# Performance work log

Hardware: AMD Instinct MI355X
Metric: run time of the kernel (lower is better)

The kernel has to match this reference:

```python
import jax, jax.numpy as jnp
import numpy as np

EPS = 1e-16
LOG_2PI = float(np.log(2.0 * np.pi))
DUMMY = -2.0 * float(np.log(10.0))  # dummy component logit / log-prob


def setup_inputs() -> dict:
    key = jax.random.key(0)
    k1, k2, k3, k4, k5 = jax.random.split(key, 5)
    B, N, V, D = 32, 1024, 512, 4
    x = jax.random.normal(k1, (B, N, D), dtype=jnp.float32)
    votes = jax.random.normal(k2, (B, V, D), dtype=jnp.float32)
    # positive stds in [0.1, 1.0)
    scales = jax.random.uniform(k3, (B, V), dtype=jnp.float32) * 0.9 + 0.1
    vote_presence_prob = jax.random.uniform(k4, (B, V), dtype=jnp.float32)
    presence = jax.random.uniform(k5, (B, N), dtype=jnp.float32)
    return {"x": x, "votes": votes, "scales": scales,
            "vote_presence_prob": vote_presence_prob,
            "presence": presence, "n_votes": 16}


def reference(x, votes, scales, vote_presence_prob, presence, n_votes):
    B, N, D = x.shape
    V = votes.shape[1]
    # Broadcast Normal log-prob: x [B,N,1,D] vs votes [B,1,V,D], scale [B,1,V,1]
    sig = scales[:, None, :, None]
    z = (x[:, :, None, :] - votes[:, None, :, :]) / sig
    lp_per_dim = -0.5 * z * z - jnp.log(sig) - 0.5 * LOG_2PI
    vote_log_prob = jnp.sum(lp_per_dim, axis=-1)                       # [B,N,V]
    vote_log_prob = jnp.concatenate(
        [vote_log_prob, jnp.full((B, N, 1), DUMMY, vote_log_prob.dtype)], axis=2)  # [B,N,V+1]

    mixing_logits = jnp.log(vote_presence_prob + EPS)                  # safe_log, [B,V]
    mixing_logits = jnp.concatenate(
        [mixing_logits, jnp.full((B, 1), DUMMY, mixing_logits.dtype)], axis=1)     # [B,V+1]
    mixing_log_prob = jax.nn.log_softmax(mixing_logits, axis=1)        # [B,V+1]

    posterior = mixing_log_prob[:, None, :] + vote_log_prob            # [B,N,V+1]
    mixture_lp_per_comp = jax.scipy.special.logsumexp(posterior, axis=2)  # [B,N]
    mixture_lp_per_comp = mixture_lp_per_comp * presence
    log_prob = jnp.sum(mixture_lp_per_comp)                            # scalar

    winning_vote_idx = jnp.argmax(posterior[:, :, :-1], axis=2)        # [B,N]
    winner = jnp.take_along_axis(votes, winning_vote_idx[:, :, None], axis=1)  # [B,N,D]
    winner_pres = jnp.take_along_axis(vote_presence_prob, winning_vote_idx, axis=1)  # [B,N]
    vote_presence = (mixing_logits[:, :-1] > mixing_logits[:, -1:]).astype(jnp.float32)  # [B,V]
    is_from_capsule = winning_vote_idx // n_votes                      # [B,N]
    posterior_mixing_probs = jax.nn.softmax(posterior, axis=-1)[..., :-1]  # [B,N,V]

    return (log_prob, vote_presence, winner, winner_pres, is_from_capsule,
            mixing_logits, mixing_log_prob, jnp.zeros_like(winner),
            jnp.zeros_like(winner_pres), posterior_mixing_probs)
```

## Files before the change

kernel.cpp:

```cpp
#include <hip/hip_runtime.h>

typedef float v2f __attribute__((ext_vector_type(2)));
typedef float v4f __attribute__((ext_vector_type(4)));

#define FEPS 1e-16f
#define LOG_2PI 1.8378770664093453f
#define DUMMYV -4.605170185988091f
#define LOG2E 1.4426950408889634f
#define LN2 0.6931471805599453f

constexpr int B = 32, N = 1024, V = 512;

constexpr long long OFF_LOGPROB    = 0;
constexpr long long OFF_VOTEPRES   = 1;
constexpr long long OFF_WINNER     = OFF_VOTEPRES + (long long)B * V;
constexpr long long OFF_WINNERPRES = OFF_WINNER + (long long)B * N * 4;
constexpr long long OFF_ISFROM     = OFF_WINNERPRES + (long long)B * N;
constexpr long long OFF_MLOGITS    = OFF_ISFROM + (long long)B * N;
constexpr long long OFF_MLOGPROB   = OFF_MLOGITS + (long long)B * (V + 1);
constexpr long long OFF_ZW         = OFF_MLOGPROB + (long long)B * (V + 1);
constexpr long long OFF_ZWP        = OFF_ZW + (long long)B * N * 4;
constexpr long long OFF_PMP        = OFF_ZWP + (long long)B * N;

__device__ __forceinline__ float fexp2(float x) {
#if __has_builtin(__builtin_amdgcn_exp2f)
    return __builtin_amdgcn_exp2f(x);
#else
    return __expf(x * LN2);
#endif
}
__device__ __forceinline__ float frcp(float x) {
#if __has_builtin(__builtin_amdgcn_rcpf)
    return __builtin_amdgcn_rcpf(x);
#else
    return 1.0f / x;
#endif
}

template<int RN> __device__ __forceinline__ float dppRorF(float x) {
    return __int_as_float(__builtin_amdgcn_update_dpp(
        0, __float_as_int(x), 0x120 | RN, 0xF, 0xF, false));
}
template<int RN> __device__ __forceinline__ int dppRorI(int x) {
    return __builtin_amdgcn_update_dpp(0, x, 0x120 | RN, 0xF, 0xF, false);
}
__device__ __forceinline__ float swz16F(float x) {
    return __int_as_float(__builtin_amdgcn_ds_swizzle(__float_as_int(x), 0x401F));
}
__device__ __forceinline__ int swz16I(int x) {
    return __builtin_amdgcn_ds_swizzle(x, 0x401F);
}

#if __has_builtin(__builtin_amdgcn_permlane32_swap)
__device__ __forceinline__ float maxSwap32(float x) {
    auto r = __builtin_amdgcn_permlane32_swap(__float_as_uint(x), __float_as_uint(x), false, false);
    return fmaxf(__uint_as_float(r[0]), __uint_as_float(r[1]));
}
__device__ __forceinline__ float sumSwap32(float x) {
    auto r = __builtin_amdgcn_permlane32_swap(__float_as_uint(x), __float_as_uint(x), false, false);
    return __uint_as_float(r[0]) + __uint_as_float(r[1]);
}
__device__ __forceinline__ int minSwap32(int x) {
    auto r = __builtin_amdgcn_permlane32_swap((unsigned)x, (unsigned)x, false, false);
    int a = (int)r[0], b = (int)r[1];
    return a < b ? a : b;
}
#else
__device__ __forceinline__ float maxSwap32(float x) { return fmaxf(x, __shfl_xor(x, 32)); }
__device__ __forceinline__ float sumSwap32(float x) { return x + __shfl_xor(x, 32); }
__device__ __forceinline__ int   minSwap32(int x)   { int o = __shfl_xor(x, 32); return o < x ? o : x; }
#endif

__device__ __forceinline__ float waveMaxF(float m) {
    m = fmaxf(m, dppRorF<1>(m));
    m = fmaxf(m, dppRorF<2>(m));
    m = fmaxf(m, dppRorF<4>(m));
    m = fmaxf(m, dppRorF<8>(m));
    m = fmaxf(m, swz16F(m));
    return maxSwap32(m);
}
__device__ __forceinline__ float waveSumF(float s) {
    s += dppRorF<1>(s);
    s += dppRorF<2>(s);
    s += dppRorF<4>(s);
    s += dppRorF<8>(s);
    s += swz16F(s);
    return sumSwap32(s);
}
__device__ __forceinline__ int waveMinI(int v) {
    int o;
    o = dppRorI<1>(v); v = o < v ? o : v;
    o = dppRorI<2>(v); v = o < v ? o : v;
    o = dppRorI<4>(v); v = o < v ? o : v;
    o = dppRorI<8>(v); v = o < v ? o : v;
    o = swz16I(v);     v = o < v ? o : v;
    return minSwap32(v);
}

__global__ __launch_bounds__(256) void k_fused(const float* __restrict__ x,
                                               const float* __restrict__ votes,
                                               const float* __restrict__ scales,
                                               const float* __restrict__ vpp,
                                               const float* __restrict__ presence,
                                               const int* __restrict__ nvp,
                                               float* __restrict__ out,
                                               float* __restrict__ ws) {
    __shared__ float s_part[4];
    const int b = blockIdx.y, t = threadIdx.x, w = t >> 6, lane = t & 63;
    const long long bV = (long long)b * V;
    const float4* votes4 = reinterpret_cast<const float4*>(votes) + bV;

    int vidx[8];
    float lg[8], lsv[8];
    float4 vt[8];
    #pragma unroll
    for (int k = 0; k < 4; ++k) {
        int v = 3 + 4 * lane + k;
        vidx[k] = v;
        vt[k]  = votes4[v];
        lsv[k] = scales[bV + v];
        lg[k]  = __logf(vpp[bV + v] + FEPS);
    }
    const int vtop[4] = {511, 0, 1, 2};
    #pragma unroll
    for (int k = 4; k < 8; ++k) {
        int v = (lane < 63) ? (259 + 4 * lane + (k - 4)) : vtop[k - 4];
        vidx[k] = v;
        vt[k]  = votes4[v];
        lsv[k] = scales[bV + v];
        lg[k]  = __logf(vpp[bV + v] + FEPS);
    }

    float mm = lg[0];
    #pragma unroll
    for (int k = 1; k < 8; ++k) mm = fmaxf(mm, lg[k]);
    float M = fmaxf(waveMaxF(mm), DUMMYV);
    float ss = 0.f;
    #pragma unroll
    for (int k = 0; k < 8; ++k) ss += __expf(lg[k] - M);
    float S = waveSumF(ss) + __expf(DUMMYV - M);
    float lse = M + __logf(S);
    float dummy_post = DUMMYV + (DUMMYV - lse);

    if (blockIdx.x == 0 && w == 0) {
        #pragma unroll
        for (int k = 0; k < 8; ++k) {
            int v = vidx[k];
            out[OFF_MLOGITS  + (long long)b * (V + 1) + v] = lg[k];
            out[OFF_MLOGPROB + (long long)b * (V + 1) + v] = lg[k] - lse;
            out[OFF_VOTEPRES + bV + v] = (lg[k] > DUMMYV) ? 1.0f : 0.0f;
        }
        if (lane == 0) {
            out[OFF_MLOGITS  + (long long)b * (V + 1) + V] = DUMMYV;
            out[OFF_MLOGPROB + (long long)b * (V + 1) + V] = DUMMYV - lse;
        }
    }

    v2f c2[4], hk[4], hvx[4], hvy[4], hvz[4], hvw[4];
    #pragma unroll
    for (int i = 0; i < 4; ++i) {
        float cc[2], kk[2], ax[2], ay[2], az[2], aw[2];
        #pragma unroll
        for (int h = 0; h < 2; ++h) {
            int k = 2 * i + h;
            float sv  = lsv[k];
            float inv = frcp(sv);
            float hh  = 0.5f * inv * inv;
            float c   = lg[k] - 4.0f * __logf(sv) - 2.0f * LOG_2PI - lse;
            float4 vv = vt[k];
            float v2  = vv.x * vv.x + vv.y * vv.y + vv.z * vv.z + vv.w * vv.w;
            cc[h] = (c - hh * v2 - dummy_post) * LOG2E;
            kk[h] = -hh * LOG2E;
            float g = 2.0f * hh * LOG2E;
            ax[h] = g * vv.x; ay[h] = g * vv.y; az[h] = g * vv.z; aw[h] = g * vv.w;
        }
        c2[i].x = cc[0];  c2[i].y = cc[1];
        hk[i].x = kk[0];  hk[i].y = kk[1];
        hvx[i].x = ax[0]; hvx[i].y = ax[1];
        hvy[i].x = ay[0]; hvy[i].y = ay[1];
        hvz[i].x = az[0]; hvz[i].y = az[1];
        hvw[i].x = aw[0]; hvw[i].y = aw[1];
    }

    const float4* x4 = reinterpret_cast<const float4*>(x) + (long long)b * N;
    int nv = nvp[0];
    float acc = 0.f;

    #pragma unroll 2
    for (int iter = 0; iter < 8; ++iter) {
        int n = blockIdx.x * 32 + iter * 4 + w;
        long long bn = (long long)b * N + n;
        float4 xv = x4[n];
        float px2 = xv.x * xv.x + xv.y * xv.y + xv.z * xv.z + xv.w * xv.w;
        v2f P2; P2.x = px2;  P2.y = px2;
        v2f Xx; Xx.x = xv.x; Xx.y = xv.x;
        v2f Xy; Xy.x = xv.y; Xy.y = xv.y;
        v2f Xz; Xz.x = xv.z; Xz.y = xv.z;
        v2f Xw; Xw.x = xv.w; Xw.y = xv.w;

        float p2s[8];
        #pragma unroll
        for (int i = 0; i < 4; ++i) {
            v2f tt = c2[i];
            tt += hk[i]  * P2;
            tt += hvx[i] * Xx;
            tt += hvy[i] * Xy;
            tt += hvz[i] * Xz;
            tt += hvw[i] * Xw;
            p2s[2 * i]     = tt.x;
            p2s[2 * i + 1] = tt.y;
        }

        float t1 = fmaxf(fmaxf(p2s[0], p2s[1]), p2s[2]);
        float t2 = fmaxf(fmaxf(p2s[3], p2s[4]), p2s[5]);
        float t3 = fmaxf(fmaxf(p2s[6], p2s[7]), t1);
        float Mrow = waveMaxF(fmaxf(t2, t3));

        int cand = 0x7fffffff;
        #pragma unroll
        for (int k = 0; k < 8; ++k)
            if (p2s[k] == Mrow && vidx[k] < cand) cand = vidx[k];
        int bi = waveMinI(cand);

        float e[8];
        float se = 0.f;
        #pragma unroll
        for (int k = 0; k < 8; ++k) { e[k] = fexp2(p2s[k]); se += e[k]; }
        se = waveSumF(se);
        float total = se + 1.0f;
        float rt = frcp(total);

        float* rp = out + OFF_PMP + bn * (long long)V;
        v4f qa; qa.x = e[0] * rt; qa.y = e[1] * rt; qa.z = e[2] * rt; qa.w = e[3] * rt;
        v4f qb; qb.x = e[4] * rt; qb.y = e[5] * rt; qb.z = e[6] * rt; qb.w = e[7] * rt;
        __builtin_nontemporal_store(qa, reinterpret_cast<v4f*>(rp + 3 + 4 * lane));
        if (lane < 63) {
            __builtin_nontemporal_store(qb, reinterpret_cast<v4f*>(rp + 259 + 4 * lane));
        } else {
            rp[511] = qb.x;
            rp[0]   = qb.y;
            v2f ez; ez.x = qb.z; ez.y = qb.w;
            *reinterpret_cast<v2f*>(rp + 1) = ez;
        }

        if (lane == 0) {
            acc += (dummy_post + LN2 * __log2f(total)) * presence[bn];
            float4 wv = votes4[bi];
            out[OFF_WINNER + bn * 4 + 0] = wv.x;
            out[OFF_WINNER + bn * 4 + 1] = wv.y;
            out[OFF_WINNER + bn * 4 + 2] = wv.z;
            out[OFF_WINNER + bn * 4 + 3] = wv.w;
            out[OFF_WINNERPRES + bn]     = vpp[bV + bi];
            out[OFF_ISFROM + bn]         = (float)((nv == 16) ? (bi >> 4) : (bi / nv));
        }
        if (lane == 1) {
            out[OFF_ZW + bn * 4 + 0] = 0.f;
            out[OFF_ZW + bn * 4 + 1] = 0.f;
            out[OFF_ZW + bn * 4 + 2] = 0.f;
            out[OFF_ZW + bn * 4 + 3] = 0.f;
            out[OFF_ZWP + bn]        = 0.f;
        }
    }

    if (lane == 0) s_part[w] = acc;
    __syncthreads();
    if (t == 0)
        ws[(long long)b * gridDim.x + blockIdx.x] =
            s_part[0] + s_part[1] + s_part[2] + s_part[3];
}

__global__ __launch_bounds__(256) void k_reduce(const float* __restrict__ ws,
                                                float* __restrict__ out, int count) {
    __shared__ float sred[256];
    int t = threadIdx.x;
    float s = 0.f;
    for (int i = t; i < count; i += 256) s += ws[i];
    sred[t] = s;
    __syncthreads();
    for (int o = 128; o > 0; o >>= 1) {
        if (t < o) sred[t] += sred[t + o];
        __syncthreads();
    }
    if (t == 0) out[OFF_LOGPROB] = sred[0];
}

extern "C" void kernel_launch(void* const* d_in, const int* in_sizes, int n_in,
                              void* d_out, int out_size, void* d_ws, size_t ws_size,
                              hipStream_t stream) {
    const float* x        = (const float*)d_in[0];
    const float* votes    = (const float*)d_in[1];
    const float* scales   = (const float*)d_in[2];
    const float* vpp      = (const float*)d_in[3];
    const float* presence = (const float*)d_in[4];
    const int*   nv       = (const int*)d_in[5];
    float* out = (float*)d_out;
    float* ws  = (float*)d_ws;

    dim3 g(N / 32, B);
    k_fused<<<g, 256, 0, stream>>>(x, votes, scales, vpp, presence, nv, out, ws);
    k_reduce<<<1, 256, 0, stream>>>(ws, out, (N / 32) * B);
}
```

Baseline: 28.17 us.

## Give each lane contiguous vote runs and use a ballot-based argmax

Each lane now owns 8 contiguous votes, rotated by 3, instead of two strided groups of 4. This lets the argmax be found with a per-lane local index, a wave ballot and one shuffle, replacing the integer wave-min reduction. Max, exp and scale are done on packed float2 vectors, the posterior stores become plain instead of nontemporal, and the zero-output stores are spread over five lanes. The presence load is hoisted, and all lanes now accumulate the log-prob term, though only lane 0's value is later read. Possible costs are slightly less coalesced store patterns per instruction and different cache behaviour from dropping the nontemporal hint.

```diff
diff --git a/kernel.cpp b/kernel.cpp
--- a/kernel.cpp
+++ b/kernel.cpp
@@ -41,14 +41,8 @@
     return __int_as_float(__builtin_amdgcn_update_dpp(
         0, __float_as_int(x), 0x120 | RN, 0xF, 0xF, false));
 }
-template<int RN> __device__ __forceinline__ int dppRorI(int x) {
-    return __builtin_amdgcn_update_dpp(0, x, 0x120 | RN, 0xF, 0xF, false);
-}
 __device__ __forceinline__ float swz16F(float x) {
     return __int_as_float(__builtin_amdgcn_ds_swizzle(__float_as_int(x), 0x401F));
-}
-__device__ __forceinline__ int swz16I(int x) {
-    return __builtin_amdgcn_ds_swizzle(x, 0x401F);
 }
 
 #if __has_builtin(__builtin_amdgcn_permlane32_swap)
@@ -60,15 +54,9 @@
     auto r = __builtin_amdgcn_permlane32_swap(__float_as_uint(x), __float_as_uint(x), false, false);
     return __uint_as_float(r[0]) + __uint_as_float(r[1]);
 }
-__device__ __forceinline__ int minSwap32(int x) {
-    auto r = __builtin_amdgcn_permlane32_swap((unsigned)x, (unsigned)x, false, false);
-    int a = (int)r[0], b = (int)r[1];
-    return a < b ? a : b;
-}
 #else
 __device__ __forceinline__ float maxSwap32(float x) { return fmaxf(x, __shfl_xor(x, 32)); }
 __device__ __forceinline__ float sumSwap32(float x) { return x + __shfl_xor(x, 32); }
-__device__ __forceinline__ int   minSwap32(int x)   { int o = __shfl_xor(x, 32); return o < x ? o : x; }
 #endif
 
 __device__ __forceinline__ float waveMaxF(float m) {
@@ -86,15 +74,6 @@
     s += dppRorF<8>(s);
     s += swz16F(s);
     return sumSwap32(s);
-}
-__device__ __forceinline__ int waveMinI(int v) {
-    int o;
-    o = dppRorI<1>(v); v = o < v ? o : v;
-    o = dppRorI<2>(v); v = o < v ? o : v;
-    o = dppRorI<4>(v); v = o < v ? o : v;
-    o = dppRorI<8>(v); v = o < v ? o : v;
-    o = swz16I(v);     v = o < v ? o : v;
-    return minSwap32(v);
 }
 
 __global__ __launch_bounds__(256) void k_fused(const float* __restrict__ x,
@@ -110,22 +89,11 @@
     const long long bV = (long long)b * V;
     const float4* votes4 = reinterpret_cast<const float4*>(votes) + bV;
 
-    int vidx[8];
     float lg[8], lsv[8];
     float4 vt[8];
     #pragma unroll
-    for (int k = 0; k < 4; ++k) {
-        int v = 3 + 4 * lane + k;
-        vidx[k] = v;
-        vt[k]  = votes4[v];
-        lsv[k] = scales[bV + v];
-        lg[k]  = __logf(vpp[bV + v] + FEPS);
-    }
-    const int vtop[4] = {511, 0, 1, 2};
-    #pragma unroll
-    for (int k = 4; k < 8; ++k) {
-        int v = (lane < 63) ? (259 + 4 * lane + (k - 4)) : vtop[k - 4];
-        vidx[k] = v;
+    for (int k = 0; k < 8; ++k) {
+        int v = (8 * lane + 3 + k) & 511;
         vt[k]  = votes4[v];
         lsv[k] = scales[bV + v];
         lg[k]  = __logf(vpp[bV + v] + FEPS);
@@ -145,7 +113,7 @@
     if (blockIdx.x == 0 && w == 0) {
         #pragma unroll
         for (int k = 0; k < 8; ++k) {
-            int v = vidx[k];
+            int v = (8 * lane + 3 + k) & 511;
             out[OFF_MLOGITS  + (long long)b * (V + 1) + v] = lg[k];
             out[OFF_MLOGPROB + (long long)b * (V + 1) + v] = lg[k] - lse;
             out[OFF_VOTEPRES + bV + v] = (lg[k] > DUMMYV) ? 1.0f : 0.0f;
@@ -191,6 +159,7 @@
         int n = blockIdx.x * 32 + iter * 4 + w;
         long long bn = (long long)b * N + n;
         float4 xv = x4[n];
+        float pres = presence[bn];
         float px2 = xv.x * xv.x + xv.y * xv.y + xv.z * xv.z + xv.w * xv.w;
         v2f P2; P2.x = px2;  P2.y = px2;
         v2f Xx; Xx.x = xv.x; Xx.y = xv.x;
@@ -198,7 +167,7 @@
         v2f Xz; Xz.x = xv.z; Xz.y = xv.z;
         v2f Xw; Xw.x = xv.w; Xw.y = xv.w;
 
-        float p2s[8];
+        v2f tt4[4];
         #pragma unroll
         for (int i = 0; i < 4; ++i) {
             v2f tt = c2[i];
@@ -207,35 +176,46 @@
             tt += hvy[i] * Xy;
             tt += hvz[i] * Xz;
             tt += hvw[i] * Xw;
-            p2s[2 * i]     = tt.x;
-            p2s[2 * i + 1] = tt.y;
-        }
-
-        float t1 = fmaxf(fmaxf(p2s[0], p2s[1]), p2s[2]);
-        float t2 = fmaxf(fmaxf(p2s[3], p2s[4]), p2s[5]);
-        float t3 = fmaxf(fmaxf(p2s[6], p2s[7]), t1);
-        float Mrow = waveMaxF(fmaxf(t2, t3));
-
-        int cand = 0x7fffffff;
-        #pragma unroll
-        for (int k = 0; k < 8; ++k)
-            if (p2s[k] == Mrow && vidx[k] < cand) cand = vidx[k];
-        int bi = waveMinI(cand);
-
-        float e[8];
-        float se = 0.f;
-        #pragma unroll
-        for (int k = 0; k < 8; ++k) { e[k] = fexp2(p2s[k]); se += e[k]; }
-        se = waveSumF(se);
+            tt4[i] = tt;
+        }
+
+        v2f m2 = __builtin_elementwise_max(
+            __builtin_elementwise_max(tt4[0], tt4[1]),
+            __builtin_elementwise_max(tt4[2], tt4[3]));
+        float m_in = fmaxf(m2.x, m2.y);
+        float Mrow = waveMaxF(m_in);
+
+        int kw = 7;
+        #pragma unroll
+        for (int k = 6; k >= 0; --k) {
+            float pv = (k & 1) ? tt4[k >> 1].y : tt4[k >> 1].x;
+            kw = (pv == m_in) ? k : kw;
+        }
+        unsigned long long bmask = __ballot(m_in == Mrow);
+        int first = (int)__builtin_ctzll(bmask);
+        int kwf = __shfl(kw, first);
+        int bi = (8 * first + 3 + kwf) & 511;
+
+        v2f ee[4];
+        #pragma unroll
+        for (int i = 0; i < 4; ++i) {
+            ee[i].x = fexp2(tt4[i].x);
+            ee[i].y = fexp2(tt4[i].y);
+        }
+        v2f s2 = (ee[0] + ee[1]) + (ee[2] + ee[3]);
+        float se = waveSumF(s2.x + s2.y);
         float total = se + 1.0f;
         float rt = frcp(total);
 
         float* rp = out + OFF_PMP + bn * (long long)V;
-        v4f qa; qa.x = e[0] * rt; qa.y = e[1] * rt; qa.z = e[2] * rt; qa.w = e[3] * rt;
-        v4f qb; qb.x = e[4] * rt; qb.y = e[5] * rt; qb.z = e[6] * rt; qb.w = e[7] * rt;
-        __builtin_nontemporal_store(qa, reinterpret_cast<v4f*>(rp + 3 + 4 * lane));
+        v2f rtv; rtv.x = rt; rtv.y = rt;
+        v2f a0 = ee[0] * rtv, a1 = ee[1] * rtv;
+        v2f b0 = ee[2] * rtv, b1 = ee[3] * rtv;
+        v4f qa; qa.x = a0.x; qa.y = a0.y; qa.z = a1.x; qa.w = a1.y;
+        v4f qb; qb.x = b0.x; qb.y = b0.y; qb.z = b1.x; qb.w = b1.y;
+        *reinterpret_cast<v4f*>(rp + 3 + 8 * lane) = qa;
         if (lane < 63) {
-            __builtin_nontemporal_store(qb, reinterpret_cast<v4f*>(rp + 259 + 4 * lane));
+            *reinterpret_cast<v4f*>(rp + 7 + 8 * lane) = qb;
         } else {
             rp[511] = qb.x;
             rp[0]   = qb.y;
@@ -243,8 +223,13 @@
             *reinterpret_cast<v2f*>(rp + 1) = ez;
         }
 
+        acc = fmaf(dummy_post + LN2 * __log2f(total), pres, acc);
+
+        if (lane < 5) {
+            long long za = (lane == 4) ? (OFF_ZWP + bn) : (OFF_ZW + bn * 4 + lane);
+            out[za] = 0.f;
+        }
         if (lane == 0) {
-            acc += (dummy_post + LN2 * __log2f(total)) * presence[bn];
             float4 wv = votes4[bi];
             out[OFF_WINNER + bn * 4 + 0] = wv.x;
             out[OFF_WINNER + bn * 4 + 1] = wv.y;
@@ -252,13 +237,6 @@
             out[OFF_WINNER + bn * 4 + 3] = wv.w;
             out[OFF_WINNERPRES + bn]     = vpp[bV + bi];
             out[OFF_ISFROM + bn]         = (float)((nv == 16) ? (bi >> 4) : (bi / nv));
-        }
-        if (lane == 1) {
-            out[OFF_ZW + bn * 4 + 0] = 0.f;
-            out[OFF_ZW + bn * 4 + 1] = 0.f;
-            out[OFF_ZW + bn * 4 + 2] = 0.f;
-            out[OFF_ZW + bn * 4 + 3] = 0.f;
-            out[OFF_ZWP + bn]        = 0.f;
         }
     }
 
```

New measurement: 32.58 us. 15.7% more time.

## Fuse final reduction via last-block atomic and stage per-vote constants in LDS

Applied to the files above, without the earlier changes.

Replaces the separate reduction kernel with a last-block-done pattern: each block writes its partial sum, increments an atomic counter, and the final block reduces all partials. The counter is reset by a memset on the stream, which replaces the second kernel launch. Per-vote constants are now computed cooperatively by all four waves (two votes per thread) and shared through LDS, instead of each wave redundantly computing all 512. The vote-to-lane mapping also changes from float4 nontemporal stores to strided coalesced scalar stores, which drops the vectorized nontemporal output path and adds extra block barriers.

```diff
diff --git a/kernel.cpp b/kernel.cpp
--- a/kernel.cpp
+++ b/kernel.cpp
@@ -1,7 +1,6 @@
 #include <hip/hip_runtime.h>
 
 typedef float v2f __attribute__((ext_vector_type(2)));
-typedef float v4f __attribute__((ext_vector_type(4)));
 
 #define FEPS 1e-16f
 #define LOG_2PI 1.8378770664093453f
@@ -10,6 +9,8 @@
 #define LN2 0.6931471805599453f
 
 constexpr int B = 32, N = 1024, V = 512;
+constexpr int GRID_X = N / 32;
+constexpr unsigned GRID_TOTAL = GRID_X * B;
 
 constexpr long long OFF_LOGPROB    = 0;
 constexpr long long OFF_VOTEPRES   = 1;
@@ -105,81 +106,84 @@
                                                const int* __restrict__ nvp,
                                                float* __restrict__ out,
                                                float* __restrict__ ws) {
-    __shared__ float s_part[4];
+    __shared__ float s_c2[512], s_hk[512], s_ax[512], s_ay[512], s_az[512], s_aw[512];
+    __shared__ float s_m[4], s_s[4], s_part[4];
+    __shared__ float sred[256];
+    __shared__ int s_last;
+
     const int b = blockIdx.y, t = threadIdx.x, w = t >> 6, lane = t & 63;
     const long long bV = (long long)b * V;
     const float4* votes4 = reinterpret_cast<const float4*>(votes) + bV;
 
-    int vidx[8];
-    float lg[8], lsv[8];
-    float4 vt[8];
-    #pragma unroll
-    for (int k = 0; k < 4; ++k) {
-        int v = 3 + 4 * lane + k;
-        vidx[k] = v;
-        vt[k]  = votes4[v];
-        lsv[k] = scales[bV + v];
-        lg[k]  = __logf(vpp[bV + v] + FEPS);
-    }
-    const int vtop[4] = {511, 0, 1, 2};
-    #pragma unroll
-    for (int k = 4; k < 8; ++k) {
-        int v = (lane < 63) ? (259 + 4 * lane + (k - 4)) : vtop[k - 4];
-        vidx[k] = v;
-        vt[k]  = votes4[v];
-        lsv[k] = scales[bV + v];
-        lg[k]  = __logf(vpp[bV + v] + FEPS);
-    }
-
-    float mm = lg[0];
-    #pragma unroll
-    for (int k = 1; k < 8; ++k) mm = fmaxf(mm, lg[k]);
-    float M = fmaxf(waveMaxF(mm), DUMMYV);
-    float ss = 0.f;
-    #pragma unroll
-    for (int k = 0; k < 8; ++k) ss += __expf(lg[k] - M);
-    float S = waveSumF(ss) + __expf(DUMMYV - M);
+    const int va = w * 128 + lane, vb = va + 64;
+    float4 v4a = votes4[va], v4b = votes4[vb];
+    float sva = scales[bV + va], svb = scales[bV + vb];
+    float lga = __logf(vpp[bV + va] + FEPS);
+    float lgb = __logf(vpp[bV + vb] + FEPS);
+
+    float mm = waveMaxF(fmaxf(lga, lgb));
+    if (lane == 0) s_m[w] = mm;
+    __syncthreads();
+    float M = fmaxf(fmaxf(fmaxf(s_m[0], s_m[1]), fmaxf(s_m[2], s_m[3])), DUMMYV);
+    float ss = waveSumF(__expf(lga - M) + __expf(lgb - M));
+    if (lane == 0) s_s[w] = ss;
+    __syncthreads();
+    float S = s_s[0] + s_s[1] + s_s[2] + s_s[3] + __expf(DUMMYV - M);
     float lse = M + __logf(S);
     float dummy_post = DUMMYV + (DUMMYV - lse);
 
-    if (blockIdx.x == 0 && w == 0) {
-        #pragma unroll
-        for (int k = 0; k < 8; ++k) {
-            int v = vidx[k];
-            out[OFF_MLOGITS  + (long long)b * (V + 1) + v] = lg[k];
-            out[OFF_MLOGPROB + (long long)b * (V + 1) + v] = lg[k] - lse;
-            out[OFF_VOTEPRES + bV + v] = (lg[k] > DUMMYV) ? 1.0f : 0.0f;
-        }
-        if (lane == 0) {
-            out[OFF_MLOGITS  + (long long)b * (V + 1) + V] = DUMMYV;
-            out[OFF_MLOGPROB + (long long)b * (V + 1) + V] = DUMMYV - lse;
-        }
-    }
+    {
+        float4 vv = v4a;
+        float inv = frcp(sva);
+        float hh = 0.5f * inv * inv;
+        float c = lga - 4.0f * __logf(sva) - 2.0f * LOG_2PI - lse;
+        float v2 = vv.x * vv.x + vv.y * vv.y + vv.z * vv.z + vv.w * vv.w;
+        int idx = ((va >> 7) << 7) + ((va & 63) << 1) + ((va >> 6) & 1);
+        float g = 2.0f * hh * LOG2E;
+        s_c2[idx] = (c - hh * v2 - dummy_post) * LOG2E;
+        s_hk[idx] = -hh * LOG2E;
+        s_ax[idx] = g * vv.x; s_ay[idx] = g * vv.y;
+        s_az[idx] = g * vv.z; s_aw[idx] = g * vv.w;
+    }
+    {
+        float4 vv = v4b;
+        float inv = frcp(svb);
+        float hh = 0.5f * inv * inv;
+        float c = lgb - 4.0f * __logf(svb) - 2.0f * LOG_2PI - lse;
+        float v2 = vv.x * vv.x + vv.y * vv.y + vv.z * vv.z + vv.w * vv.w;
+        int idx = ((vb >> 7) << 7) + ((vb & 63) << 1) + ((vb >> 6) & 1);
+        float g = 2.0f * hh * LOG2E;
+        s_c2[idx] = (c - hh * v2 - dummy_post) * LOG2E;
+        s_hk[idx] = -hh * LOG2E;
+        s_ax[idx] = g * vv.x; s_ay[idx] = g * vv.y;
+        s_az[idx] = g * vv.z; s_aw[idx] = g * vv.w;
+    }
+
+    if (blockIdx.x == 0) {
+        long long mb = (long long)b * (V + 1);
+        out[OFF_MLOGITS  + mb + va] = lga;
+        out[OFF_MLOGITS  + mb + vb] = lgb;
+        out[OFF_MLOGPROB + mb + va] = lga - lse;
+        out[OFF_MLOGPROB + mb + vb] = lgb - lse;
+        out[OFF_VOTEPRES + bV + va] = (lga > DUMMYV) ? 1.0f : 0.0f;
+        out[OFF_VOTEPRES + bV + vb] = (lgb > DUMMYV) ? 1.0f : 0.0f;
+        if (t == 0) {
+            out[OFF_MLOGITS  + mb + V] = DUMMYV;
+            out[OFF_MLOGPROB + mb + V] = DUMMYV - lse;
+        }
+    }
+    __syncthreads();
 
     v2f c2[4], hk[4], hvx[4], hvy[4], hvz[4], hvw[4];
     #pragma unroll
     for (int i = 0; i < 4; ++i) {
-        float cc[2], kk[2], ax[2], ay[2], az[2], aw[2];
-        #pragma unroll
-        for (int h = 0; h < 2; ++h) {
-            int k = 2 * i + h;
-            float sv  = lsv[k];
-            float inv = frcp(sv);
-            float hh  = 0.5f * inv * inv;
-            float c   = lg[k] - 4.0f * __logf(sv) - 2.0f * LOG_2PI - lse;
-            float4 vv = vt[k];
-            float v2  = vv.x * vv.x + vv.y * vv.y + vv.z * vv.z + vv.w * vv.w;
-            cc[h] = (c - hh * v2 - dummy_post) * LOG2E;
-            kk[h] = -hh * LOG2E;
-            float g = 2.0f * hh * LOG2E;
-            ax[h] = g * vv.x; ay[h] = g * vv.y; az[h] = g * vv.z; aw[h] = g * vv.w;
-        }
-        c2[i].x = cc[0];  c2[i].y = cc[1];
-        hk[i].x = kk[0];  hk[i].y = kk[1];
-        hvx[i].x = ax[0]; hvx[i].y = ax[1];
-        hvy[i].x = ay[0]; hvy[i].y = ay[1];
-        hvz[i].x = az[0]; hvz[i].y = az[1];
-        hvw[i].x = aw[0]; hvw[i].y = aw[1];
+        int o = i * 128 + lane * 2;
+        c2[i]  = *reinterpret_cast<const v2f*>(&s_c2[o]);
+        hk[i]  = *reinterpret_cast<const v2f*>(&s_hk[o]);
+        hvx[i] = *reinterpret_cast<const v2f*>(&s_ax[o]);
+        hvy[i] = *reinterpret_cast<const v2f*>(&s_ay[o]);
+        hvz[i] = *reinterpret_cast<const v2f*>(&s_az[o]);
+        hvw[i] = *reinterpret_cast<const v2f*>(&s_aw[o]);
     }
 
     const float4* x4 = reinterpret_cast<const float4*>(x) + (long long)b * N;
@@ -219,7 +223,7 @@
         int cand = 0x7fffffff;
         #pragma unroll
         for (int k = 0; k < 8; ++k)
-            if (p2s[k] == Mrow && vidx[k] < cand) cand = vidx[k];
+            if (p2s[k] == Mrow && (k * 64 + lane) < cand) cand = k * 64 + lane;
         int bi = waveMinI(cand);
 
         float e[8];
@@ -230,18 +234,10 @@
         float total = se + 1.0f;
         float rt = frcp(total);
 
-        float* rp = out + OFF_PMP + bn * (long long)V;
-        v4f qa; qa.x = e[0] * rt; qa.y = e[1] * rt; qa.z = e[2] * rt; qa.w = e[3] * rt;
-        v4f qb; qb.x = e[4] * rt; qb.y = e[5] * rt; qb.z = e[6] * rt; qb.w = e[7] * rt;
-        __builtin_nontemporal_store(qa, reinterpret_cast<v4f*>(rp + 3 + 4 * lane));
-        if (lane < 63) {
-            __builtin_nontemporal_store(qb, reinterpret_cast<v4f*>(rp + 259 + 4 * lane));
-        } else {
-            rp[511] = qb.x;
-            rp[0]   = qb.y;
-            v2f ez; ez.x = qb.z; ez.y = qb.w;
-            *reinterpret_cast<v2f*>(rp + 1) = ez;
-        }
+        long long pb = OFF_PMP + bn * (long long)V;
+        #pragma unroll
+        for (int k = 0; k < 8; ++k)
+            out[pb + k * 64 + lane] = e[k] * rt;
 
         if (lane == 0) {
             acc += (dummy_post + LN2 * __log2f(total)) * presence[bn];
@@ -264,24 +260,29 @@
 
     if (lane == 0) s_part[w] = acc;
     __syncthreads();
-    if (t == 0)
-        ws[(long long)b * gridDim.x + blockIdx.x] =
-            s_part[0] + s_part[1] + s_part[2] + s_part[3];
-}
-
-__global__ __launch_bounds__(256) void k_reduce(const float* __restrict__ ws,
-                                                float* __restrict__ out, int count) {
-    __shared__ float sred[256];
-    int t = threadIdx.x;
-    float s = 0.f;
-    for (int i = t; i < count; i += 256) s += ws[i];
-    sred[t] = s;
-    __syncthreads();
-    for (int o = 128; o > 0; o >>= 1) {
-        if (t < o) sred[t] += sred[t + o];
+    if (t == 0) {
+        float p = s_part[0] + s_part[1] + s_part[2] + s_part[3];
+        ws[(long long)b * GRID_X + blockIdx.x] = p;
+        __threadfence();
+        unsigned old = __hip_atomic_fetch_add(
+            reinterpret_cast<unsigned*>(ws + GRID_TOTAL), 1u,
+            __ATOMIC_ACQ_REL, __HIP_MEMORY_SCOPE_AGENT);
+        s_last = (old == GRID_TOTAL - 1);
+    }
+    __syncthreads();
+    if (s_last) {
+        __threadfence();
+        float s = 0.f;
+        for (int i = t; i < (int)GRID_TOTAL; i += 256)
+            s += __hip_atomic_load(&ws[i], __ATOMIC_RELAXED, __HIP_MEMORY_SCOPE_AGENT);
+        sred[t] = s;
         __syncthreads();
-    }
-    if (t == 0) out[OFF_LOGPROB] = sred[0];
+        for (int o = 128; o > 0; o >>= 1) {
+            if (t < o) sred[t] += sred[t + o];
+            __syncthreads();
+        }
+        if (t == 0) out[OFF_LOGPROB] = sred[0];
+    }
 }
 
 extern "C" void kernel_launch(void* const* d_in, const int* in_sizes, int n_in,
@@ -296,7 +297,8 @@
     float* out = (float*)d_out;
     float* ws  = (float*)d_ws;
 
-    dim3 g(N / 32, B);
+    hipMemsetAsync((void*)(ws + GRID_TOTAL), 0, sizeof(unsigned), stream);
+
+    dim3 g(GRID_X, B);
     k_fused<<<g, 256, 0, stream>>>(x, votes, scales, vpp, presence, nv, out, ws);
-    k_reduce<<<1, 256, 0, stream>>>(ws, out, (N / 32) * B);
-}
+}
```

Result: slower. 98.96 us (+251.3%).

## Use strided vote-to-lane mapping with scalar stores and 64 rows per block

Applied to the files above, without the earlier changes.

Replaces the offset, misaligned 4-wide vote assignment per lane with a simple lane+64*k mapping. Posterior probability stores become eight coalesced scalar dword stores per row instead of unaligned 16-byte nontemporal vector stores with a special case for the last lane. The block also processes 64 rows instead of 32, halving the grid and the number of per-block setup passes and partial sums. In exchange the stores lose the nontemporal hint and vector width, and fewer blocks are launched.

```diff
diff --git a/kernel.cpp b/kernel.cpp
--- a/kernel.cpp
+++ b/kernel.cpp
@@ -1,7 +1,6 @@
 #include <hip/hip_runtime.h>
 
 typedef float v2f __attribute__((ext_vector_type(2)));
-typedef float v4f __attribute__((ext_vector_type(4)));
 
 #define FEPS 1e-16f
 #define LOG_2PI 1.8378770664093453f
@@ -10,6 +9,8 @@
 #define LN2 0.6931471805599453f
 
 constexpr int B = 32, N = 1024, V = 512;
+constexpr int ROWS_PER_BLOCK = 64;
+constexpr int GRID_X = N / ROWS_PER_BLOCK;
 
 constexpr long long OFF_LOGPROB    = 0;
 constexpr long long OFF_VOTEPRES   = 1;
@@ -110,22 +111,11 @@
     const long long bV = (long long)b * V;
     const float4* votes4 = reinterpret_cast<const float4*>(votes) + bV;
 
-    int vidx[8];
     float lg[8], lsv[8];
     float4 vt[8];
     #pragma unroll
-    for (int k = 0; k < 4; ++k) {
-        int v = 3 + 4 * lane + k;
-        vidx[k] = v;
-        vt[k]  = votes4[v];
-        lsv[k] = scales[bV + v];
-        lg[k]  = __logf(vpp[bV + v] + FEPS);
-    }
-    const int vtop[4] = {511, 0, 1, 2};
-    #pragma unroll
-    for (int k = 4; k < 8; ++k) {
-        int v = (lane < 63) ? (259 + 4 * lane + (k - 4)) : vtop[k - 4];
-        vidx[k] = v;
+    for (int k = 0; k < 8; ++k) {
+        int v = k * 64 + lane;
         vt[k]  = votes4[v];
         lsv[k] = scales[bV + v];
         lg[k]  = __logf(vpp[bV + v] + FEPS);
@@ -145,7 +135,7 @@
     if (blockIdx.x == 0 && w == 0) {
         #pragma unroll
         for (int k = 0; k < 8; ++k) {
-            int v = vidx[k];
+            int v = k * 64 + lane;
             out[OFF_MLOGITS  + (long long)b * (V + 1) + v] = lg[k];
             out[OFF_MLOGPROB + (long long)b * (V + 1) + v] = lg[k] - lse;
             out[OFF_VOTEPRES + bV + v] = (lg[k] > DUMMYV) ? 1.0f : 0.0f;
@@ -187,8 +177,8 @@
     float acc = 0.f;
 
     #pragma unroll 2
-    for (int iter = 0; iter < 8; ++iter) {
-        int n = blockIdx.x * 32 + iter * 4 + w;
+    for (int iter = 0; iter < ROWS_PER_BLOCK / 4; ++iter) {
+        int n = blockIdx.x * ROWS_PER_BLOCK + iter * 4 + w;
         long long bn = (long long)b * N + n;
         float4 xv = x4[n];
         float px2 = xv.x * xv.x + xv.y * xv.y + xv.z * xv.z + xv.w * xv.w;
@@ -219,7 +209,7 @@
         int cand = 0x7fffffff;
         #pragma unroll
         for (int k = 0; k < 8; ++k)
-            if (p2s[k] == Mrow && vidx[k] < cand) cand = vidx[k];
+            if (p2s[k] == Mrow && (k * 64 + lane) < cand) cand = k * 64 + lane;
         int bi = waveMinI(cand);
 
         float e[8];
@@ -230,18 +220,10 @@
         float total = se + 1.0f;
         float rt = frcp(total);
 
-        float* rp = out + OFF_PMP + bn * (long long)V;
-        v4f qa; qa.x = e[0] * rt; qa.y = e[1] * rt; qa.z = e[2] * rt; qa.w = e[3] * rt;
-        v4f qb; qb.x = e[4] * rt; qb.y = e[5] * rt; qb.z = e[6] * rt; qb.w = e[7] * rt;
-        __builtin_nontemporal_store(qa, reinterpret_cast<v4f*>(rp + 3 + 4 * lane));
-        if (lane < 63) {
-            __builtin_nontemporal_store(qb, reinterpret_cast<v4f*>(rp + 259 + 4 * lane));
-        } else {
-            rp[511] = qb.x;
-            rp[0]   = qb.y;
-            v2f ez; ez.x = qb.z; ez.y = qb.w;
-            *reinterpret_cast<v2f*>(rp + 1) = ez;
-        }
+        long long pb = OFF_PMP + bn * (long long)V;
+        #pragma unroll
+        for (int k = 0; k < 8; ++k)
+            out[pb + k * 64 + lane] = e[k] * rt;
 
         if (lane == 0) {
             acc += (dummy_post + LN2 * __log2f(total)) * presence[bn];
@@ -296,7 +278,7 @@
     float* out = (float*)d_out;
     float* ws  = (float*)d_ws;
 
-    dim3 g(N / 32, B);
+    dim3 g(GRID_X, B);
     k_fused<<<g, 256, 0, stream>>>(x, votes, scales, vpp, presence, nv, out, ws);
-    k_reduce<<<1, 256, 0, stream>>>(ws, out, (N / 32) * B);
-}
+    k_reduce<<<1, 256, 0, stream>>>(ws, out, GRID_X * B);
+}
```

After: 31.02 us. 10.1% more time.
